# Kernel optimization log

Measured on AMD Instinct MI355X. Metric: run time of the kernel, lower is better.

## Reference

```python
import jax, jax.numpy as jnp
import numpy as np

P, N, GRID, C, S, STEPS, N_ADJ = 128, 512, 112, 64, 128, 3, 4
HW = GRID * GRID
IN_DIM = C + 2


def _ring_adjacency():
    # prepare_gcn_component builds a ring graph: each vertex connected to
    # n_adj nearest neighbors along the polygon, row-normalized.
    offs = np.concatenate([np.arange(1, N_ADJ // 2 + 1), -np.arange(1, N_ADJ // 2 + 1)])
    A = np.zeros((N, N), np.float32)
    idx = np.arange(N)
    for o in offs:
        A[idx, (idx + o) % N] = 1.0
    A /= A.sum(1, keepdims=True)
    return jnp.asarray(A)


def setup_inputs() -> dict:
    key = jax.random.key(0)
    ks = jax.random.split(key, 10)
    std = 0.01  # matches m.weight.data.normal_(0.0, 0.01)
    return {
        "feature": jax.random.normal(ks[0], (P, HW, C), jnp.float32),
        "init_polys": jax.random.uniform(ks[1], (P, N, 2), jnp.float32),
        "adj": _ring_adjacency(),
        "W1s": jax.random.normal(ks[2], (STEPS, IN_DIM, S), jnp.float32) * std,
        "W1n": jax.random.normal(ks[3], (STEPS, IN_DIM, S), jnp.float32) * std,
        "b1": jnp.zeros((STEPS, S), jnp.float32),
        "W2s": jax.random.normal(ks[4], (STEPS, S, S), jnp.float32) * std,
        "W2n": jax.random.normal(ks[5], (STEPS, S, S), jnp.float32) * std,
        "b2": jnp.zeros((STEPS, S), jnp.float32),
        "Wfc": jax.random.normal(ks[6], (STEPS, S, 2), jnp.float32) * std,
        "bfc": jnp.zeros((STEPS, 2), jnp.float32),
    }


def _gather(feat, ids):
    # feat: [P, HW, C], ids: [P, N] int -> [P, N, C]
    return jnp.take_along_axis(feat, ids[:, :, None], axis=1)


def _nearest_sample(feature, poly):
    # step-0 `sampling` path: gather at floor(coord*grid) flat indices
    X0 = jnp.clip(jnp.floor(poly[..., 0] * GRID), 0, GRID - 1)
    Y0 = jnp.clip(jnp.floor(poly[..., 1] * GRID), 0, GRID - 1)
    ids = (X0 + Y0 * GRID).astype(jnp.int32)
    return _gather(feature, ids)


def _interpolated_sum(feature, poly):
    Xs = poly[..., 0] * GRID
    Ys = poly[..., 1] * GRID
    X0 = jnp.floor(Xs); X1 = X0 + 1.0
    Y0 = jnp.floor(Ys); Y1 = Y0 + 1.0
    w00 = (X1 - Xs) * (Y1 - Ys)
    w01 = (X1 - Xs) * (Ys - Y0)
    w10 = (Xs - X0) * (Y1 - Ys)
    w11 = (Xs - X0) * (Ys - Y0)
    X0c = jnp.clip(X0, 0, GRID - 1).astype(jnp.int32)
    X1c = jnp.clip(X1, 0, GRID - 1).astype(jnp.int32)
    Y0c = jnp.clip(Y0, 0, GRID - 1).astype(jnp.int32)
    Y1c = jnp.clip(Y1, 0, GRID - 1).astype(jnp.int32)
    M00 = _gather(feature, X0c + Y0c * GRID)
    M01 = _gather(feature, X0c + Y1c * GRID)
    M10 = _gather(feature, X1c + Y0c * GRID)
    M11 = _gather(feature, X1c + Y1c * GRID)
    return (w00[..., None] * M00 + w01[..., None] * M01 +
            w10[..., None] * M10 + w11[..., None] * M11)


def _gconv(x, adj, Ws, Wn, b):
    # x: [P, N, D]; adj: [N, N] (shared ring graph)
    nbr = jnp.einsum('nm,pmd->pnd', adj, x)
    return x @ Ws + nbr @ Wn + b


def _gcn(x, adj, i, W1s, W1n, b1, W2s, W2n, b2, Wfc, bfc):
    h = jax.nn.relu(_gconv(x, adj, W1s[i], W1n[i], b1[i]))
    h = jax.nn.relu(_gconv(h, adj, W2s[i], W2n[i], b2[i]))
    return h @ Wfc[i] + bfc[i]  # [P, N, 2]


def reference(feature, init_polys, adj, W1s, W1n, b1, W2s, W2n, b2, Wfc, bfc):
    poly = init_polys
    for i in range(STEPS):
        cnn_feat = _nearest_sample(feature, poly) if i == 0 else _interpolated_sum(feature, poly)
        inp = jnp.concatenate([cnn_feat, poly], axis=2)  # [P, N, C+2]
        pred = _gcn(inp, adj, i, W1s, W1n, b1, W2s, W2n, b2, Wfc, bfc)
        poly = poly + pred
    return poly
```

## Files before the change

kernel.cpp:

```cpp
#include <hip/hip_runtime.h>

#define P_      128
#define NV      512
#define GRID_   112
#define HW_     (GRID_*GRID_)
#define C_      64
#define S_      128
#define IN_DIM_ 66

typedef short bf16x8 __attribute__((ext_vector_type(8)));
typedef float f32x4  __attribute__((ext_vector_type(4)));

__device__ __forceinline__ unsigned short f2bf(float x) {
    union { float f; unsigned int u; } v; v.f = x;
    unsigned int r = (v.u + 0x7FFFu + ((v.u >> 16) & 1u)) >> 16;
    return (unsigned short)r;
}
__device__ __forceinline__ float2 up2(unsigned int u) {
    union { unsigned int u; float f; } a, b;
    a.u = u << 16; b.u = u & 0xFFFF0000u;
    return make_float2(a.f, b.f);
}
__device__ __forceinline__ unsigned int pk2(float lo, float hi) {
    return (unsigned int)f2bf(lo) | ((unsigned int)f2bf(hi) << 16);
}

__global__ __launch_bounds__(256) void wprep_kernel(
    const float* __restrict__ W1s, const float* __restrict__ W1n,
    const float* __restrict__ W2s, const float* __restrict__ W2n,
    unsigned short* __restrict__ W1p, unsigned short* __restrict__ W2p)
{
    int idx = blockIdx.x * 256 + threadIdx.x;
    const int N1 = 3 * 5 * 8 * 64 * 8;
    const int N2 = 3 * 8 * 8 * 64 * 8;
    if (idx < N1) {
        int j = idx & 7, lane = (idx >> 3) & 63, nt = (idx >> 9) & 7;
        int ks = (idx >> 12) % 5, step = idx / 20480;
        int n = nt * 16 + (lane & 15);
        int k = ks * 32 + (lane >> 4) * 8 + j;
        float v = 0.f;
        if (k < 66)       v = W1s[(step * 66 + k) * 128 + n];
        else if (k < 132) v = W1n[(step * 66 + (k - 66)) * 128 + n];
        W1p[idx] = f2bf(v);
    } else if (idx < N1 + N2) {
        int e = idx - N1;
        int j = e & 7, lane = (e >> 3) & 63, nt = (e >> 9) & 7;
        int ks = (e >> 12) & 7, step = e >> 15;
        int n = nt * 16 + (lane & 15);
        int k = ks * 32 + (lane >> 4) * 8 + j;
        float v = (k < 128) ? W2s[(step * 128 + k) * 128 + n]
                            : W2n[(step * 128 + (k - 128)) * 128 + n];
        W2p[e] = f2bf(v);
    }
}

__global__ __launch_bounds__(256) void sample_kernel(
    const float* __restrict__ feature, const float* __restrict__ poly,
    unsigned short* __restrict__ inp, int nearest)
{
    int w = threadIdx.x >> 6, lane = threadIdx.x & 63;
    int g = blockIdx.x * 4 + w;
    int p = g >> 9;
    float px = poly[2 * g], py = poly[2 * g + 1];
    const float* fb = feature + (size_t)p * HW_ * C_;
    float val;
    if (nearest) {
        float X0 = fminf(fmaxf(floorf(px * (float)GRID_), 0.f), (float)(GRID_ - 1));
        float Y0 = fminf(fmaxf(floorf(py * (float)GRID_), 0.f), (float)(GRID_ - 1));
        int id = (int)X0 + (int)Y0 * GRID_;
        val = fb[(size_t)id * C_ + lane];
    } else {
        float Xs = px * (float)GRID_, Ys = py * (float)GRID_;
        float X0 = floorf(Xs), Y0 = floorf(Ys);
        float X1 = X0 + 1.f, Y1 = Y0 + 1.f;
        float ax = X1 - Xs, bx = Xs - X0;
        float ay = Y1 - Ys, by = Ys - Y0;
        int X0c = (int)fminf(fmaxf(X0, 0.f), (float)(GRID_ - 1));
        int X1c = (int)fminf(fmaxf(X1, 0.f), (float)(GRID_ - 1));
        int Y0c = (int)fminf(fmaxf(Y0, 0.f), (float)(GRID_ - 1));
        int Y1c = (int)fminf(fmaxf(Y1, 0.f), (float)(GRID_ - 1));
        float m00 = fb[(size_t)(X0c + Y0c * GRID_) * C_ + lane];
        float m01 = fb[(size_t)(X0c + Y1c * GRID_) * C_ + lane];
        float m10 = fb[(size_t)(X1c + Y0c * GRID_) * C_ + lane];
        float m11 = fb[(size_t)(X1c + Y1c * GRID_) * C_ + lane];
        val = (ax * ay) * m00 + (ax * by) * m01 + (bx * ay) * m10 + (bx * by) * m11;
    }
    unsigned short* row = inp + (size_t)g * 72;
    row[lane] = f2bf(val);
    if (lane < 8) {
        float v2 = (lane == 0) ? px : (lane == 1) ? py : 0.f;
        row[64 + lane] = f2bf(v2);
    }
}

__global__ __launch_bounds__(256) void gemm1_kernel(
    const unsigned short* __restrict__ inp,
    const unsigned short* __restrict__ W1p,
    const float* __restrict__ b1,
    unsigned short* __restrict__ h1)
{
    __shared__ __align__(16) unsigned int As[64 * 84];
    int p = blockIdx.x >> 3, n0 = (blockIdx.x & 7) * 64;
    const unsigned int* inpu = (const unsigned int*)(inp + (size_t)p * NV * 72);

    for (int idx = threadIdx.x; idx < 64 * 84; idx += 256) {
        int r = idx / 84, u = idx - r * 84;
        unsigned int val;
        if (u < 33) {
            val = inpu[(n0 + r) * 36 + u];
        } else if (u < 66) {
            int uu = u - 33;
            unsigned int a = inpu[((n0 + r - 2) & 511) * 36 + uu];
            unsigned int b = inpu[((n0 + r - 1) & 511) * 36 + uu];
            unsigned int c = inpu[((n0 + r + 1) & 511) * 36 + uu];
            unsigned int d = inpu[((n0 + r + 2) & 511) * 36 + uu];
            float2 fa = up2(a), fb = up2(b), fc = up2(c), fd = up2(d);
            val = pk2(0.25f * (fa.x + fb.x + fc.x + fd.x),
                      0.25f * (fa.y + fb.y + fc.y + fd.y));
        } else val = 0u;
        As[idx] = val;
    }
    __syncthreads();

    int wv = threadIdx.x >> 6, lane = threadIdx.x & 63;
    int m = lane & 15, q = lane >> 4;
    const unsigned short* Asrow = (const unsigned short*)As + (wv * 16 + m) * 168 + q * 8;
    f32x4 acc[8];
    #pragma unroll
    for (int nt = 0; nt < 8; nt++) acc[nt] = (f32x4){0.f, 0.f, 0.f, 0.f};
    const bf16x8* Bp = (const bf16x8*)W1p;
    for (int ks = 0; ks < 5; ks++) {
        bf16x8 a = *(const bf16x8*)(Asrow + ks * 32);
        #pragma unroll
        for (int nt = 0; nt < 8; nt++) {
            bf16x8 b = Bp[(ks * 8 + nt) * 64 + lane];
            acc[nt] = __builtin_amdgcn_mfma_f32_16x16x32_bf16(a, b, acc[nt], 0, 0, 0);
        }
    }
    unsigned short* h1b = h1 + ((size_t)p * NV + n0) * 128;
    #pragma unroll
    for (int nt = 0; nt < 8; nt++) {
        int col = nt * 16 + m;
        float bias = b1[col];
        #pragma unroll
        for (int rg = 0; rg < 4; rg++) {
            int row = wv * 16 + q * 4 + rg;
            h1b[row * 128 + col] = f2bf(fmaxf(acc[nt][rg] + bias, 0.f));
        }
    }
}

__global__ __launch_bounds__(256) void gemm2fc_kernel(
    const unsigned short* __restrict__ h1,
    const unsigned short* __restrict__ W2p,
    const float* __restrict__ b2,
    const float* __restrict__ Wfc, const float* __restrict__ bfc,
    const float* __restrict__ poly_in, float* __restrict__ poly_out)
{
    __shared__ __align__(16) char smem[64 * 132 * 4 + 68 * 64 * 4];
    unsigned int* As2 = (unsigned int*)smem;
    unsigned int* raw = (unsigned int*)(smem + 64 * 132 * 4);
    float* h2 = (float*)smem;

    int p = blockIdx.x >> 3, n0 = (blockIdx.x & 7) * 64;
    const unsigned int* h1u = (const unsigned int*)h1 + (size_t)p * NV * 64;

    for (int idx = threadIdx.x; idx < 68 * 64; idx += 256) {
        int r = idx >> 6, u = idx & 63;
        raw[idx] = h1u[(size_t)((n0 + r - 2) & 511) * 64 + u];
    }
    __syncthreads();
    for (int idx = threadIdx.x; idx < 64 * 132; idx += 256) {
        int r = idx / 132, u = idx - r * 132;
        unsigned int val;
        if (u < 64) val = raw[(r + 2) * 64 + u];
        else if (u < 128) {
            int uu = u - 64;
            float2 fa = up2(raw[r * 64 + uu]),       fb = up2(raw[(r + 1) * 64 + uu]);
            float2 fc = up2(raw[(r + 3) * 64 + uu]), fd = up2(raw[(r + 4) * 64 + uu]);
            val = pk2(0.25f * (fa.x + fb.x + fc.x + fd.x),
                      0.25f * (fa.y + fb.y + fc.y + fd.y));
        } else val = 0u;
        As2[idx] = val;
    }
    __syncthreads();

    int wv = threadIdx.x >> 6, lane = threadIdx.x & 63;
    int m = lane & 15, q = lane >> 4;
    const unsigned short* Asrow = (const unsigned short*)As2 + (wv * 16 + m) * 264 + q * 8;
    f32x4 acc[8];
    #pragma unroll
    for (int nt = 0; nt < 8; nt++) acc[nt] = (f32x4){0.f, 0.f, 0.f, 0.f};
    const bf16x8* Bp = (const bf16x8*)W2p;
    for (int ks = 0; ks < 8; ks++) {
        bf16x8 a = *(const bf16x8*)(Asrow + ks * 32);
        #pragma unroll
        for (int nt = 0; nt < 8; nt++) {
            bf16x8 b = Bp[(ks * 8 + nt) * 64 + lane];
            acc[nt] = __builtin_amdgcn_mfma_f32_16x16x32_bf16(a, b, acc[nt], 0, 0, 0);
        }
    }
    __syncthreads();
    #pragma unroll
    for (int nt = 0; nt < 8; nt++) {
        int col = nt * 16 + m;
        float bias = b2[col];
        #pragma unroll
        for (int rg = 0; rg < 4; rg++) {
            int row = wv * 16 + q * 4 + rg;
            h2[row * 129 + col] = fmaxf(acc[nt][rg] + bias, 0.f);
        }
    }
    __syncthreads();
    if (threadIdx.x < 128) {
        int v = threadIdx.x >> 1, j = threadIdx.x & 1;
        float pr = bfc[j];
        const float* hv = h2 + v * 129;
        for (int c = 0; c < 128; c++) pr += hv[c] * Wfc[c * 2 + j];
        size_t o = ((size_t)p * NV + n0 + v) * 2 + j;
        poly_out[o] = poly_in[o] + pr;
    }
}

extern "C" void kernel_launch(void* const* d_in, const int* in_sizes, int n_in,
                              void* d_out, int out_size, void* d_ws, size_t ws_size,
                              hipStream_t stream)
{
    const float* feature    = (const float*)d_in[0];
    const float* init_polys = (const float*)d_in[1];
    const float* W1s = (const float*)d_in[3];
    const float* W1n = (const float*)d_in[4];
    const float* b1  = (const float*)d_in[5];
    const float* W2s = (const float*)d_in[6];
    const float* W2n = (const float*)d_in[7];
    const float* b2  = (const float*)d_in[8];
    const float* Wfc = (const float*)d_in[9];
    const float* bfc = (const float*)d_in[10];
    float* out = (float*)d_out;

    char* wsb = (char*)d_ws;
    float* polyA = (float*)wsb;                  wsb += (size_t)131072 * 4;
    float* polyB = (float*)wsb;                  wsb += (size_t)131072 * 4;
    unsigned short* W1p = (unsigned short*)wsb;  wsb += (size_t)61440 * 2;
    unsigned short* W2p = (unsigned short*)wsb;  wsb += (size_t)98304 * 2;
    unsigned short* inp = (unsigned short*)wsb;  wsb += (size_t)P_ * NV * 72 * 2;
    unsigned short* h1  = (unsigned short*)wsb;  wsb += (size_t)P_ * NV * 128 * 2;

    wprep_kernel<<<624, 256, 0, stream>>>(W1s, W1n, W2s, W2n, W1p, W2p);

    const float* pin = init_polys;
    for (int i = 0; i < 3; i++) {
        float* pout = (i == 2) ? out : ((i == 0) ? polyA : polyB);
        sample_kernel<<<P_ * NV / 4, 256, 0, stream>>>(feature, pin, inp, i == 0);
        gemm1_kernel<<<P_ * 8, 256, 0, stream>>>(
            inp, W1p + (size_t)i * 20480, b1 + i * 128, h1);
        gemm2fc_kernel<<<P_ * 8, 256, 0, stream>>>(
            h1, W2p + (size_t)i * 32768, b2 + i * 128,
            Wfc + i * 256, bfc + i * 2, pin, pout);
        pin = pout;
    }
}
```

Baseline: 656.1 us.

## Fuse sampling, both graph convolutions and FC into one per-step kernel

Merges the sample, gemm1 and gemm2fc kernels into a single step kernel. Each block recomputes a halo of ring neighbours (84 sampled rows, 80 h1 rows) so the intermediate inp and h1 tensors stay in shared memory and no longer round-trip through global memory. Two launches per step are removed as well. The cost is redundant sampling and GEMM1 work on the halo rows, plus higher shared-memory use per block (about 72 KB), which may lower occupancy.

```diff
diff --git a/kernel.cpp b/kernel.cpp
--- a/kernel.cpp
+++ b/kernel.cpp
@@ -6,7 +6,6 @@
 #define HW_     (GRID_*GRID_)
 #define C_      64
 #define S_      128
-#define IN_DIM_ 66
 
 typedef short bf16x8 __attribute__((ext_vector_type(8)));
 typedef float f32x4  __attribute__((ext_vector_type(4)));
@@ -54,153 +53,146 @@
     }
 }
 
-__global__ __launch_bounds__(256) void sample_kernel(
-    const float* __restrict__ feature, const float* __restrict__ poly,
-    unsigned short* __restrict__ inp, int nearest)
-{
-    int w = threadIdx.x >> 6, lane = threadIdx.x & 63;
-    int g = blockIdx.x * 4 + w;
-    int p = g >> 9;
-    float px = poly[2 * g], py = poly[2 * g + 1];
-    const float* fb = feature + (size_t)p * HW_ * C_;
-    float val;
-    if (nearest) {
-        float X0 = fminf(fmaxf(floorf(px * (float)GRID_), 0.f), (float)(GRID_ - 1));
-        float Y0 = fminf(fmaxf(floorf(py * (float)GRID_), 0.f), (float)(GRID_ - 1));
-        int id = (int)X0 + (int)Y0 * GRID_;
-        val = fb[(size_t)id * C_ + lane];
-    } else {
-        float Xs = px * (float)GRID_, Ys = py * (float)GRID_;
-        float X0 = floorf(Xs), Y0 = floorf(Ys);
-        float X1 = X0 + 1.f, Y1 = Y0 + 1.f;
-        float ax = X1 - Xs, bx = Xs - X0;
-        float ay = Y1 - Ys, by = Ys - Y0;
-        int X0c = (int)fminf(fmaxf(X0, 0.f), (float)(GRID_ - 1));
-        int X1c = (int)fminf(fmaxf(X1, 0.f), (float)(GRID_ - 1));
-        int Y0c = (int)fminf(fmaxf(Y0, 0.f), (float)(GRID_ - 1));
-        int Y1c = (int)fminf(fmaxf(Y1, 0.f), (float)(GRID_ - 1));
-        float m00 = fb[(size_t)(X0c + Y0c * GRID_) * C_ + lane];
-        float m01 = fb[(size_t)(X0c + Y1c * GRID_) * C_ + lane];
-        float m10 = fb[(size_t)(X1c + Y0c * GRID_) * C_ + lane];
-        float m11 = fb[(size_t)(X1c + Y1c * GRID_) * C_ + lane];
-        val = (ax * ay) * m00 + (ax * by) * m01 + (bx * ay) * m10 + (bx * by) * m11;
-    }
-    unsigned short* row = inp + (size_t)g * 72;
-    row[lane] = f2bf(val);
-    if (lane < 8) {
-        float v2 = (lane == 0) ? px : (lane == 1) ? py : 0.f;
-        row[64 + lane] = f2bf(v2);
-    }
-}
-
-__global__ __launch_bounds__(256) void gemm1_kernel(
-    const unsigned short* __restrict__ inp,
+#define X_BYTES 38976
+#define Y_BYTES 33792
+__global__ __launch_bounds__(256) void step_kernel(
+    const float* __restrict__ feature,
+    const float* __restrict__ poly_in,
     const unsigned short* __restrict__ W1p,
     const float* __restrict__ b1,
-    unsigned short* __restrict__ h1)
-{
-    __shared__ __align__(16) unsigned int As[64 * 84];
-    int p = blockIdx.x >> 3, n0 = (blockIdx.x & 7) * 64;
-    const unsigned int* inpu = (const unsigned int*)(inp + (size_t)p * NV * 72);
-
-    for (int idx = threadIdx.x; idx < 64 * 84; idx += 256) {
-        int r = idx / 84, u = idx - r * 84;
-        unsigned int val;
-        if (u < 33) {
-            val = inpu[(n0 + r) * 36 + u];
-        } else if (u < 66) {
-            int uu = u - 33;
-            unsigned int a = inpu[((n0 + r - 2) & 511) * 36 + uu];
-            unsigned int b = inpu[((n0 + r - 1) & 511) * 36 + uu];
-            unsigned int c = inpu[((n0 + r + 1) & 511) * 36 + uu];
-            unsigned int d = inpu[((n0 + r + 2) & 511) * 36 + uu];
-            float2 fa = up2(a), fb = up2(b), fc = up2(c), fd = up2(d);
-            val = pk2(0.25f * (fa.x + fb.x + fc.x + fd.x),
-                      0.25f * (fa.y + fb.y + fc.y + fd.y));
-        } else val = 0u;
-        As[idx] = val;
-    }
-    __syncthreads();
-
-    int wv = threadIdx.x >> 6, lane = threadIdx.x & 63;
-    int m = lane & 15, q = lane >> 4;
-    const unsigned short* Asrow = (const unsigned short*)As + (wv * 16 + m) * 168 + q * 8;
-    f32x4 acc[8];
-    #pragma unroll
-    for (int nt = 0; nt < 8; nt++) acc[nt] = (f32x4){0.f, 0.f, 0.f, 0.f};
-    const bf16x8* Bp = (const bf16x8*)W1p;
-    for (int ks = 0; ks < 5; ks++) {
-        bf16x8 a = *(const bf16x8*)(Asrow + ks * 32);
-        #pragma unroll
-        for (int nt = 0; nt < 8; nt++) {
-            bf16x8 b = Bp[(ks * 8 + nt) * 64 + lane];
-            acc[nt] = __builtin_amdgcn_mfma_f32_16x16x32_bf16(a, b, acc[nt], 0, 0, 0);
-        }
-    }
-    unsigned short* h1b = h1 + ((size_t)p * NV + n0) * 128;
-    #pragma unroll
-    for (int nt = 0; nt < 8; nt++) {
-        int col = nt * 16 + m;
-        float bias = b1[col];
-        #pragma unroll
-        for (int rg = 0; rg < 4; rg++) {
-            int row = wv * 16 + q * 4 + rg;
-            h1b[row * 128 + col] = f2bf(fmaxf(acc[nt][rg] + bias, 0.f));
-        }
-    }
-}
-
-__global__ __launch_bounds__(256) void gemm2fc_kernel(
-    const unsigned short* __restrict__ h1,
     const unsigned short* __restrict__ W2p,
     const float* __restrict__ b2,
     const float* __restrict__ Wfc, const float* __restrict__ bfc,
-    const float* __restrict__ poly_in, float* __restrict__ poly_out)
+    float* __restrict__ poly_out,
+    int nearest)
 {
-    __shared__ __align__(16) char smem[64 * 132 * 4 + 68 * 64 * 4];
-    unsigned int* As2 = (unsigned int*)smem;
-    unsigned int* raw = (unsigned int*)(smem + 64 * 132 * 4);
-    float* h2 = (float*)smem;
-
-    int p = blockIdx.x >> 3, n0 = (blockIdx.x & 7) * 64;
-    const unsigned int* h1u = (const unsigned int*)h1 + (size_t)p * NV * 64;
-
-    for (int idx = threadIdx.x; idx < 68 * 64; idx += 256) {
-        int r = idx >> 6, u = idx & 63;
-        raw[idx] = h1u[(size_t)((n0 + r - 2) & 511) * 64 + u];
-    }
-    __syncthreads();
-    for (int idx = threadIdx.x; idx < 64 * 132; idx += 256) {
-        int r = idx / 132, u = idx - r * 132;
-        unsigned int val;
-        if (u < 64) val = raw[(r + 2) * 64 + u];
-        else if (u < 128) {
-            int uu = u - 64;
-            float2 fa = up2(raw[r * 64 + uu]),       fb = up2(raw[(r + 1) * 64 + uu]);
-            float2 fc = up2(raw[(r + 3) * 64 + uu]), fd = up2(raw[(r + 4) * 64 + uu]);
-            val = pk2(0.25f * (fa.x + fb.x + fc.x + fd.x),
-                      0.25f * (fa.y + fb.y + fc.y + fd.y));
-        } else val = 0u;
-        As2[idx] = val;
-    }
-    __syncthreads();
-
+    __shared__ __align__(16) char smem[X_BYTES + Y_BYTES];
+    unsigned int*   raw_u = (unsigned int*)smem;
+    unsigned int*   A1_u  = (unsigned int*)(smem + 12096);
+    unsigned short* h1s   = (unsigned short*)smem;
+    unsigned int*   A2_u  = (unsigned int*)(smem + X_BYTES);
+    float*          h2    = (float*)(smem + X_BYTES);
+
+    int p  = blockIdx.x >> 3;
+    int n0 = (blockIdx.x & 7) * 64;
     int wv = threadIdx.x >> 6, lane = threadIdx.x & 63;
     int m = lane & 15, q = lane >> 4;
-    const unsigned short* Asrow = (const unsigned short*)As2 + (wv * 16 + m) * 264 + q * 8;
-    f32x4 acc[8];
-    #pragma unroll
-    for (int nt = 0; nt < 8; nt++) acc[nt] = (f32x4){0.f, 0.f, 0.f, 0.f};
-    const bf16x8* Bp = (const bf16x8*)W2p;
+
+    const float* fb = feature + (size_t)p * HW_ * C_;
+    const float* pp = poly_in + (size_t)p * NV * 2;
+    for (int r = wv; r < 84; r += 4) {
+        int n = (n0 + r - 10) & (NV - 1);
+        float px = pp[2 * n], py = pp[2 * n + 1];
+        float val;
+        if (nearest) {
+            float X0 = fminf(fmaxf(floorf(px * (float)GRID_), 0.f), (float)(GRID_ - 1));
+            float Y0 = fminf(fmaxf(floorf(py * (float)GRID_), 0.f), (float)(GRID_ - 1));
+            int id = (int)X0 + (int)Y0 * GRID_;
+            val = fb[(size_t)id * C_ + lane];
+        } else {
+            float Xs = px * (float)GRID_, Ys = py * (float)GRID_;
+            float X0 = floorf(Xs), Y0 = floorf(Ys);
+            float X1 = X0 + 1.f, Y1 = Y0 + 1.f;
+            float ax = X1 - Xs, bx = Xs - X0;
+            float ay = Y1 - Ys, by = Ys - Y0;
+            int X0c = (int)fminf(fmaxf(X0, 0.f), (float)(GRID_ - 1));
+            int X1c = (int)fminf(fmaxf(X1, 0.f), (float)(GRID_ - 1));
+            int Y0c = (int)fminf(fmaxf(Y0, 0.f), (float)(GRID_ - 1));
+            int Y1c = (int)fminf(fmaxf(Y1, 0.f), (float)(GRID_ - 1));
+            float m00 = fb[(size_t)(X0c + Y0c * GRID_) * C_ + lane];
+            float m01 = fb[(size_t)(X0c + Y1c * GRID_) * C_ + lane];
+            float m10 = fb[(size_t)(X1c + Y0c * GRID_) * C_ + lane];
+            float m11 = fb[(size_t)(X1c + Y1c * GRID_) * C_ + lane];
+            val = (ax * ay) * m00 + (ax * by) * m01 + (bx * ay) * m10 + (bx * by) * m11;
+        }
+        unsigned short* row = (unsigned short*)raw_u + r * 72;
+        row[lane] = f2bf(val);
+        if (lane < 8)
+            row[64 + lane] = (lane == 0) ? f2bf(px) : (lane == 1) ? f2bf(py) : 0;
+    }
+    __syncthreads();
+
+    for (int idx = threadIdx.x; idx < 80 * 84; idx += 256) {
+        int a = idx / 84, u = idx - a * 84;
+        unsigned int val;
+        if (u < 33) {
+            val = raw_u[(a + 2) * 36 + u];
+        } else if (u < 66) {
+            int uu = u - 33;
+            float2 fa = up2(raw_u[a * 36 + uu]),       fb2 = up2(raw_u[(a + 1) * 36 + uu]);
+            float2 fc = up2(raw_u[(a + 3) * 36 + uu]), fd  = up2(raw_u[(a + 4) * 36 + uu]);
+            val = pk2(0.25f * (fa.x + fb2.x + fc.x + fd.x),
+                      0.25f * (fa.y + fb2.y + fc.y + fd.y));
+        } else val = 0u;
+        A1_u[idx] = val;
+    }
+    __syncthreads();
+
+    f32x4 acc1[10];
+    #pragma unroll
+    for (int i = 0; i < 10; i++) acc1[i] = (f32x4){0.f, 0.f, 0.f, 0.f};
+    const bf16x8* B1 = (const bf16x8*)W1p;
+    #pragma unroll
+    for (int i = 0; i < 10; i++) {
+        int t = wv * 10 + i;
+        int mt = t >> 3, nt = t & 7;
+        const unsigned short* arow = (const unsigned short*)A1_u + (mt * 16 + m) * 168 + q * 8;
+        #pragma unroll
+        for (int ks = 0; ks < 5; ks++) {
+            bf16x8 a = *(const bf16x8*)(arow + ks * 32);
+            bf16x8 b = B1[(ks * 8 + nt) * 64 + lane];
+            acc1[i] = __builtin_amdgcn_mfma_f32_16x16x32_bf16(a, b, acc1[i], 0, 0, 0);
+        }
+    }
+    __syncthreads();
+
+    #pragma unroll
+    for (int i = 0; i < 10; i++) {
+        int t = wv * 10 + i;
+        int mt = t >> 3, nt = t & 7;
+        int col = nt * 16 + m;
+        float bias = b1[col];
+        #pragma unroll
+        for (int rg = 0; rg < 4; rg++) {
+            int row = mt * 16 + q * 4 + rg;
+            h1s[row * 132 + col] = f2bf(fmaxf(acc1[i][rg] + bias, 0.f));
+        }
+    }
+    __syncthreads();
+
+    const unsigned int* h1u = (const unsigned int*)h1s;
+    for (int idx = threadIdx.x; idx < 64 * 128; idx += 256) {
+        int a = idx >> 7, u = idx & 127;
+        unsigned int val;
+        if (u < 64) {
+            val = h1u[(a + 8) * 66 + u];
+        } else {
+            int uu = u - 64;
+            float2 fa = up2(h1u[(a + 6) * 66 + uu]), fb2 = up2(h1u[(a + 7) * 66 + uu]);
+            float2 fc = up2(h1u[(a + 9) * 66 + uu]), fd  = up2(h1u[(a + 10) * 66 + uu]);
+            val = pk2(0.25f * (fa.x + fb2.x + fc.x + fd.x),
+                      0.25f * (fa.y + fb2.y + fc.y + fd.y));
+        }
+        A2_u[(a * 132) + u] = val;
+    }
+    __syncthreads();
+
+    f32x4 acc2[8];
+    #pragma unroll
+    for (int nt = 0; nt < 8; nt++) acc2[nt] = (f32x4){0.f, 0.f, 0.f, 0.f};
+    const bf16x8* B2 = (const bf16x8*)W2p;
+    const unsigned short* arow2 = (const unsigned short*)A2_u + (wv * 16 + m) * 264 + q * 8;
+    #pragma unroll
     for (int ks = 0; ks < 8; ks++) {
-        bf16x8 a = *(const bf16x8*)(Asrow + ks * 32);
+        bf16x8 a = *(const bf16x8*)(arow2 + ks * 32);
         #pragma unroll
         for (int nt = 0; nt < 8; nt++) {
-            bf16x8 b = Bp[(ks * 8 + nt) * 64 + lane];
-            acc[nt] = __builtin_amdgcn_mfma_f32_16x16x32_bf16(a, b, acc[nt], 0, 0, 0);
-        }
-    }
-    __syncthreads();
+            bf16x8 b = B2[(ks * 8 + nt) * 64 + lane];
+            acc2[nt] = __builtin_amdgcn_mfma_f32_16x16x32_bf16(a, b, acc2[nt], 0, 0, 0);
+        }
+    }
+    __syncthreads();
+
     #pragma unroll
     for (int nt = 0; nt < 8; nt++) {
         int col = nt * 16 + m;
@@ -208,14 +200,16 @@
         #pragma unroll
         for (int rg = 0; rg < 4; rg++) {
             int row = wv * 16 + q * 4 + rg;
-            h2[row * 129 + col] = fmaxf(acc[nt][rg] + bias, 0.f);
-        }
-    }
-    __syncthreads();
+            h2[row * 129 + col] = fmaxf(acc2[nt][rg] + bias, 0.f);
+        }
+    }
+    __syncthreads();
+
     if (threadIdx.x < 128) {
         int v = threadIdx.x >> 1, j = threadIdx.x & 1;
         float pr = bfc[j];
         const float* hv = h2 + v * 129;
+        #pragma unroll 4
         for (int c = 0; c < 128; c++) pr += hv[c] * Wfc[c * 2 + j];
         size_t o = ((size_t)p * NV + n0 + v) * 2 + j;
         poly_out[o] = poly_in[o] + pr;
@@ -239,24 +233,22 @@
     float* out = (float*)d_out;
 
     char* wsb = (char*)d_ws;
-    float* polyA = (float*)wsb;                  wsb += (size_t)131072 * 4;
-    float* polyB = (float*)wsb;                  wsb += (size_t)131072 * 4;
+    float* polyA = (float*)wsb;                  wsb += (size_t)P_ * NV * 2 * 4;
+    float* polyB = (float*)wsb;                  wsb += (size_t)P_ * NV * 2 * 4;
     unsigned short* W1p = (unsigned short*)wsb;  wsb += (size_t)61440 * 2;
-    unsigned short* W2p = (unsigned short*)wsb;  wsb += (size_t)98304 * 2;
-    unsigned short* inp = (unsigned short*)wsb;  wsb += (size_t)P_ * NV * 72 * 2;
-    unsigned short* h1  = (unsigned short*)wsb;  wsb += (size_t)P_ * NV * 128 * 2;
+    unsigned short* W2p = (unsigned short*)wsb;
 
     wprep_kernel<<<624, 256, 0, stream>>>(W1s, W1n, W2s, W2n, W1p, W2p);
 
     const float* pin = init_polys;
     for (int i = 0; i < 3; i++) {
         float* pout = (i == 2) ? out : ((i == 0) ? polyA : polyB);
-        sample_kernel<<<P_ * NV / 4, 256, 0, stream>>>(feature, pin, inp, i == 0);
-        gemm1_kernel<<<P_ * 8, 256, 0, stream>>>(
-            inp, W1p + (size_t)i * 20480, b1 + i * 128, h1);
-        gemm2fc_kernel<<<P_ * 8, 256, 0, stream>>>(
-            h1, W2p + (size_t)i * 32768, b2 + i * 128,
-            Wfc + i * 256, bfc + i * 2, pin, pout);
+        step_kernel<<<P_ * 8, 256, 0, stream>>>(
+            feature, pin,
+            W1p + (size_t)i * 20480, b1 + i * 128,
+            W2p + (size_t)i * 32768, b2 + i * 128,
+            Wfc + i * 256, bfc + i * 2,
+            pout, i == 0);
         pin = pout;
     }
 }
```

Measured after the change: 699.9 us. 6.7% more time.
